# Kernel optimization log

Measured on AMD Instinct MI355X. Metric: run time of the kernel, lower is better.

## Reference

```python
import jax, jax.numpy as jnp
import numpy as np

B, NQ, NK = 4, 1024, 1024
DQ, DK, DO = 1024, 1024, 1024
H = 16
HIDDEN = 2048  # mlp_ratio=2.0


def dyt(x, alpha, gamma):
    # DyT: gamma * tanh(alpha * x), gamma broadcast over last (channel) dim for 3D input
    return gamma[None, None, :] * jnp.tanh(alpha * x)


def setup_inputs() -> dict:
    key = jax.random.key(0)
    ks = jax.random.split(key, 12)
    s = lambda d: 1.0 / np.sqrt(d)
    return {
        "xk": jax.random.normal(ks[0], (B, NK, DK), jnp.float32),
        "xq": jax.random.normal(ks[1], (B, NQ, DQ), jnp.float32),
        "alpha_q": jnp.float32(0.5), "gamma_q": jnp.ones((DQ,), jnp.float32),
        "alpha_k": jnp.float32(0.5), "gamma_k": jnp.ones((DK,), jnp.float32),
        "Wq": jax.random.normal(ks[2], (DQ, DO), jnp.float32) * s(DQ),
        "Wkv": jax.random.normal(ks[3], (DK, 2 * DO), jnp.float32) * s(DK),
        "Wproj": jax.random.normal(ks[4], (DO, DO), jnp.float32) * s(DO),
        "bproj": jnp.zeros((DO,), jnp.float32),
        "alpha2": jnp.float32(0.5), "gamma2": jnp.ones((DO,), jnp.float32),
        "W1": jax.random.normal(ks[5], (DO, HIDDEN), jnp.float32) * s(DO),
        "b1": jnp.zeros((HIDDEN,), jnp.float32),
        "W2": jax.random.normal(ks[6], (HIDDEN, DO), jnp.float32) * s(HIDDEN),
        "b2": jnp.zeros((DO,), jnp.float32),
    }


def reference(xk, xq, alpha_q, gamma_q, alpha_k, gamma_k, Wq, Wkv, Wproj, bproj,
              alpha2, gamma2, W1, b1, W2, b2):
    head_dim = DO // H
    scale = head_dim ** -0.5
    # DyT pre-norms
    xk_n = dyt(xk, alpha_k, gamma_k)
    xq_n = dyt(xq, alpha_q, gamma_q)
    # projections (qkv_bias=False)
    q = (xq_n @ Wq).reshape(B, NQ, H, head_dim)          # bqhd
    kv = (xk_n @ Wkv).reshape(B, NK, 2, H, head_dim)
    k, v = kv[:, :, 0], kv[:, :, 1]                       # bkhd
    attn = jax.nn.softmax(jnp.einsum('bqhd,bkhd->bhqk', q, k) * scale, axis=-1)
    o = jnp.einsum('bhqk,bkhd->bqhd', attn, v).reshape(B, NQ, DO)
    x = o @ Wproj + bproj
    # MLP with residual (drop_path/dropout are identity in eval)
    h = dyt(x, alpha2, gamma2)
    h = jax.nn.gelu(h @ W1 + b1, approximate=False)
    h = h @ W2 + b2
    return x + h
```

## Files before the change

### kernel.cpp

```cpp
#include <hip/hip_runtime.h>
#include <hip/hip_fp16.h>
#include <cstdint>

typedef _Float16 f16x8 __attribute__((ext_vector_type(8)));
typedef _Float16 f16x4 __attribute__((ext_vector_type(4)));
typedef float    f32x4 __attribute__((ext_vector_type(4)));
typedef float    f32x16 __attribute__((ext_vector_type(16)));

__device__ __forceinline__ f32x4 mfma16(f16x8 a, f16x8 b, f32x4 c) {
  return __builtin_amdgcn_mfma_f32_16x16x32_f16(a, b, c, 0, 0, 0);
}
__device__ __forceinline__ f32x16 mfma32(f16x8 a, f16x8 b, f32x16 c) {
  return __builtin_amdgcn_mfma_f32_32x32x16_f16(a, b, c, 0, 0, 0);
}
__device__ __forceinline__ void gload_lds16(const void* g, void* l) {
  __builtin_amdgcn_global_load_lds(
      (const __attribute__((address_space(1))) void*)g,
      (__attribute__((address_space(3))) void*)l, 16, 0, 0);
}
__device__ __forceinline__ unsigned pkrtz(float a, float b) {
  auto h2 = __builtin_amdgcn_cvt_pkrtz(a, b);
  return __builtin_bit_cast(unsigned, h2);
}

__device__ __forceinline__ void wtrans_tile256(
    const float* __restrict__ S, _Float16* __restrict__ D,
    int R, int C, int bx, int by, float sc, float* tle )
{
  int tx = threadIdx.x & 31, ty = threadIdx.x >> 5;
  int x = bx * 32 + tx;
#pragma unroll
  for (int j = 0; j < 4; ++j) {
    int y = by * 32 + ty + j * 8;
    tle[(ty + j * 8) * 33 + tx] = S[(size_t)y * C + x];
  }
  __syncthreads();
  int xo = by * 32 + tx;
#pragma unroll
  for (int j = 0; j < 4; ++j) {
    int yo = bx * 32 + ty + j * 8;
    D[(size_t)yo * R + xo] = (_Float16)(tle[tx * 33 + ty + j * 8] * sc);
  }
}

__global__ __launch_bounds__(256) void prep_kernel(
    const float* __restrict__ Xq, const float* __restrict__ Xk,
    const float* __restrict__ aq, const float* __restrict__ gq,
    const float* __restrict__ ak, const float* __restrict__ gk,
    _Float16* __restrict__ Yq, _Float16* __restrict__ Yk,
    const float* __restrict__ Wq, const float* __restrict__ Wkv,
    _Float16* __restrict__ WqT, _Float16* __restrict__ WkvT)
{
  if (blockIdx.x < 8192) {
    int i = blockIdx.x * 256 + threadIdx.x;
    const float* X; const float* gamma; float a; _Float16* Y;
    if (i < 1048576) { X = Xq; gamma = gq; a = aq[0]; Y = Yq; }
    else { i -= 1048576; X = Xk; gamma = gk; a = ak[0]; Y = Yk; }
    float4 v = ((const float4*)X)[i];
    int c = (i * 4) & 1023;
    f16x4 o;
    o[0] = (_Float16)(gamma[c + 0] * tanhf(a * v.x));
    o[1] = (_Float16)(gamma[c + 1] * tanhf(a * v.y));
    o[2] = (_Float16)(gamma[c + 2] * tanhf(a * v.z));
    o[3] = (_Float16)(gamma[c + 3] * tanhf(a * v.w));
    *(f16x4*)(Y + (size_t)i * 4) = o;
  } else {
    __shared__ float tle[32 * 33];
    int t = blockIdx.x - 8192;
    const float* S; _Float16* D; int R, C; float sc = 1.0f;
    if (t < 1024)      { S = Wq;  D = WqT;  R = 1024; C = 1024; sc = 0.18033688011112042f; }
    else               { S = Wkv; D = WkvT; R = 1024; C = 2048; t -= 1024; }
    const int tilesX = C >> 5;
    wtrans_tile256(S, D, R, C, t % tilesX, t / tilesX, sc, tle);
  }
}

template <int EPI>
__device__ __forceinline__ void gemm_body(
    _Float16* smem,
    const _Float16* __restrict__ A, const _Float16* __restrict__ BT,
    int N, int K, int bm, int bn,
    _Float16* __restrict__ C16, _Float16* __restrict__ X16,
    const float* __restrict__ bias, const float* __restrict__ alpha_p,
    const float* __restrict__ gamma, const _Float16* __restrict__ resid16,
    float* __restrict__ outf)
{
  const int tid = threadIdx.x;
  const int w = tid >> 6, l = tid & 63;
  const int g = l >> 4, r = l & 15;
  const int wm = w >> 1, wn = w & 1;
  const int srow = tid >> 2;
  const int skey = (tid >> 3) & 3;
  const int scol = ((tid & 3) ^ skey) << 3;

  const _Float16* gA = A + (size_t)(bm + srow) * K + scol;
  const _Float16* gB = BT + (size_t)(bn + srow) * K + scol;
  char* dA = (char*)smem + tid * 16;
  char* dB = (char*)smem + 8192 + tid * 16;

  const int rk = (r >> 1) & 3;
  const int gsw = (g ^ rk) << 3;

  f32x4 acc[2][4] = {};
  const int KT = K >> 5;

  auto stage = [&](int buf) {
    gload_lds16(gA, dA + buf * 16384);
    gload_lds16(gB, dB + buf * 16384);
    gA += 32; gB += 32;
  };

  stage(0);
  stage(1);

  int cur = 0;
  for (int kt = 0; kt < KT; ++kt) {
    if (kt < KT - 1) asm volatile("s_waitcnt vmcnt(2) lgkmcnt(0)" ::: "memory");
    else             asm volatile("s_waitcnt vmcnt(0) lgkmcnt(0)" ::: "memory");
    __builtin_amdgcn_s_barrier();
    asm volatile("" ::: "memory");
    if (kt + 2 < KT) { int b2 = cur + 2; if (b2 >= 3) b2 -= 3; stage(b2); }
    const _Float16* Asc = smem + cur * 8192;
    const _Float16* Bsc = Asc + 4096;
    f16x8 af[2], bf[4];
#pragma unroll
    for (int m = 0; m < 2; ++m)
      af[m] = *(const f16x8*)(Asc + (wm * 32 + m * 16 + r) * 32 + gsw);
#pragma unroll
    for (int n = 0; n < 4; ++n)
      bf[n] = *(const f16x8*)(Bsc + (wn * 64 + n * 16 + r) * 32 + gsw);
    __builtin_amdgcn_s_setprio(1);
#pragma unroll
    for (int m = 0; m < 2; ++m)
#pragma unroll
      for (int n = 0; n < 4; ++n)
        acc[m][n] = mfma16(af[m], bf[n], acc[m][n]);
    __builtin_amdgcn_s_setprio(0);
    ++cur; if (cur == 3) cur = 0;
  }

  const int row0 = bm + wm * 32 + 4 * g;
  const int col0 = bn + wn * 64 + r;

  if constexpr (EPI == 5) {
    if (bn < 1024) {
#pragma unroll
      for (int m = 0; m < 2; ++m)
#pragma unroll
        for (int n = 0; n < 4; ++n)
#pragma unroll
          for (int rr = 0; rr < 4; ++rr)
            C16[(size_t)(row0 + m * 16 + rr) * 1024 + col0 + n * 16] =
                (_Float16)acc[m][n][rr];
    } else {
#pragma unroll
      for (int m = 0; m < 2; ++m) {
        const int row = row0 + m * 16;
        const int bq = row >> 10, nk = row & 1023;
#pragma unroll
        for (int n = 0; n < 4; ++n) {
          const int vcol = col0 + n * 16 - 1024;
          f16x4 t;
#pragma unroll
          for (int rr = 0; rr < 4; ++rr) t[rr] = (_Float16)acc[m][n][rr];
          *(f16x4*)(X16 + ((size_t)((bq << 4) + (vcol >> 6)) * 64 + (vcol & 63)) * 1024 + nk) = t;
        }
      }
    }
    return;
  }

#pragma unroll
  for (int m = 0; m < 2; ++m) {
#pragma unroll
    for (int n = 0; n < 4; ++n) {
#pragma unroll
      for (int rr = 0; rr < 4; ++rr) {
        const int row = row0 + m * 16 + rr;
        const int col = col0 + n * 16;
        const size_t idx = (size_t)row * N + col;
        float v = acc[m][n][rr];
        if constexpr (EPI == 0) {
          C16[idx] = (_Float16)v;
        } else if constexpr (EPI == 2) {
          float x = v + bias[col];
          X16[idx] = (_Float16)x;
          C16[idx] = (_Float16)(gamma[col] * tanhf(alpha_p[0] * x));
        } else if constexpr (EPI == 3) {
          float tt = v + bias[col];
          C16[idx] = (_Float16)(0.5f * tt * (1.0f + erff(tt * 0.7071067811865475f)));
        } else {
          outf[idx] = (float)resid16[idx] + v + bias[col];
        }
      }
    }
  }
}

template <int EPI>
__global__ __launch_bounds__(512, 6) void gemm_f16(
    const _Float16* __restrict__ A, const _Float16* __restrict__ BT,
    int N, int K, int nTnShift,
    _Float16* __restrict__ C16, _Float16* __restrict__ X16,
    const float* __restrict__ bias, const float* __restrict__ alpha_p,
    const float* __restrict__ gamma, const _Float16* __restrict__ resid16,
    float* __restrict__ outf)
{
  __shared__ __align__(16) _Float16 smem[24576];
  const int chunk = gridDim.x >> 3;
  const int bid = ((int)blockIdx.x & 7) * chunk + ((int)blockIdx.x >> 3);
  const int bm = (bid >> nTnShift) << 7;
  const int bn = (bid & ((1 << nTnShift) - 1)) << 7;
  gemm_body<EPI>(smem, A, BT, N, K, bm, bn,
                 C16, X16, bias, alpha_p, gamma, resid16, outf);
}

__global__ __launch_bounds__(512, 6) void gemm_qkv(
    const _Float16* __restrict__ Aq, const _Float16* __restrict__ Bq,
    _Float16* __restrict__ Cq,
    const _Float16* __restrict__ Ak, const _Float16* __restrict__ Bk,
    _Float16* __restrict__ K16, _Float16* __restrict__ VT)
{
  __shared__ __align__(16) _Float16 smem[24576];
  int bid = ((int)blockIdx.x & 7) * 96 + ((int)blockIdx.x >> 3);
  if (bid < 256) {
    gemm_body<0>(smem, Aq, Bq, 1024, 1024, (bid >> 3) << 7, (bid & 7) << 7,
                 Cq, nullptr, nullptr, nullptr, nullptr, nullptr, nullptr);
  } else {
    bid -= 256;
    gemm_body<5>(smem, Ak, Bk, 2048, 1024, (bid >> 4) << 7, (bid & 15) << 7,
                 K16, VT, nullptr, nullptr, nullptr, nullptr, nullptr);
  }
}

__global__ __launch_bounds__(256) void attn_kernel(
    const _Float16* __restrict__ Q, const _Float16* __restrict__ K16,
    const _Float16* __restrict__ VT, _Float16* __restrict__ O,
    const float* __restrict__ Wproj, const float* __restrict__ W1,
    const float* __restrict__ W2,
    _Float16* __restrict__ WprojT, _Float16* __restrict__ W1T,
    _Float16* __restrict__ W2T)
{
  __shared__ __align__(16) char smemc[65536];

  const int tid = threadIdx.x;

  if (blockIdx.x >= 512) {
    int t = blockIdx.x - 512;
    const float* S; _Float16* D; int R, C;
    if (t < 1024)      { S = Wproj; D = WprojT; R = 1024; C = 1024; }
    else if (t < 3072) { S = W1;    D = W1T;    R = 1024; C = 2048; t -= 1024; }
    else               { S = W2;    D = W2T;    R = 2048; C = 1024; t -= 3072; }
    const int tilesX = C >> 5;
    wtrans_tile256(S, D, R, C, t % tilesX, t / tilesX, 1.0f, (float*)smemc);
    return;
  }

  const int bid = ((int)blockIdx.x & 7) * 64 + ((int)blockIdx.x >> 3);
  const int qb = bid & 7, hh = (bid >> 3) & 15, b = bid >> 7;
  const int w = tid >> 6, l = tid & 63;
  const int r = l & 31, h2 = l >> 5;
  const int q0 = qb * 128 + w * 32;

  f16x8 qf[4];
  {
    const _Float16* qp = Q + (size_t)(b * 1024 + q0 + r) * 1024 + hh * 64 + 8 * h2;
#pragma unroll
    for (int s = 0; s < 4; ++s) qf[s] = *(const f16x8*)(qp + s * 16);
  }

  f32x16 oacc0 = {}, oacc1 = {};
  float rl0 = 0.f, rl1 = 0.f, rl2 = 0.f, rl3 = 0.f;

  const int srow = tid >> 3, sslot = tid & 7;
  const int swz = (sslot ^ (srow & 7)) << 3;
  const _Float16* kbase = K16 + (size_t)(b * 1024 + srow) * 1024 + hh * 64 + swz;
  const _Float16* vbase = VT + ((size_t)((b * 16 + hh) * 64) + srow) * 1024 + swz;
  char* kd0 = (char*)smemc + tid * 16;
  char* vd0 = (char*)smemc + 8192 + tid * 16;

  auto stage = [&](int t) {
    const size_t kb = (size_t)(t << 6);
    const int buf = t & 3;
    char* kd = kd0 + buf * 16384;
    char* vd = vd0 + buf * 16384;
#pragma unroll
    for (int j = 0; j < 2; ++j)
      gload_lds16(kbase + (kb + 32 * j) * 1024, kd + j * 4096);
#pragma unroll
    for (int j = 0; j < 2; ++j)
      gload_lds16(vbase + (size_t)(32 * j) * 1024 + kb, vd + j * 4096);
  };

  stage(0);
  stage(1);

  const int rsw0 = r & 7;

  for (int kt = 0; kt < 16; ++kt) {
    if (kt + 2 < 16) stage(kt + 2);
    if (kt < 14)       asm volatile("s_waitcnt vmcnt(8)" ::: "memory");
    else if (kt == 14) asm volatile("s_waitcnt vmcnt(4)" ::: "memory");
    else               asm volatile("s_waitcnt vmcnt(0)" ::: "memory");
    __builtin_amdgcn_s_barrier();
    asm volatile("" ::: "memory");

    const _Float16* Kc = (const _Float16*)(smemc + (kt & 3) * 16384);
    const _Float16* Vc = Kc + 4096;

    f32x16 s0 = {}, s1 = {};
    __builtin_amdgcn_s_setprio(1);
#pragma unroll
    for (int s = 0; s < 4; ++s) {
      const int cch = 2 * s + h2;
      f16x8 a0 = *(const f16x8*)(Kc + r * 64 + ((cch ^ rsw0) << 3));
      f16x8 a1 = *(const f16x8*)(Kc + (32 + r) * 64 + ((cch ^ rsw0) << 3));
      s0 = mfma32(a0, qf[s], s0);
      s1 = mfma32(a1, qf[s], s1);
    }
    __builtin_amdgcn_s_setprio(0);

#pragma unroll
    for (int i = 0; i < 16; i += 4) {
      s0[i]   = __builtin_amdgcn_exp2f(s0[i]);   rl0 += s0[i];
      s0[i+1] = __builtin_amdgcn_exp2f(s0[i+1]); rl1 += s0[i+1];
      s0[i+2] = __builtin_amdgcn_exp2f(s0[i+2]); rl2 += s0[i+2];
      s0[i+3] = __builtin_amdgcn_exp2f(s0[i+3]); rl3 += s0[i+3];
    }
#pragma unroll
    for (int i = 0; i < 16; i += 4) {
      s1[i]   = __builtin_amdgcn_exp2f(s1[i]);   rl0 += s1[i];
      s1[i+1] = __builtin_amdgcn_exp2f(s1[i+1]); rl1 += s1[i+1];
      s1[i+2] = __builtin_amdgcn_exp2f(s1[i+2]); rl2 += s1[i+2];
      s1[i+3] = __builtin_amdgcn_exp2f(s1[i+3]); rl3 += s1[i+3];
    }

    unsigned own[16];
#pragma unroll
    for (int u = 0; u < 8; ++u) {
      const int tb = (u & 3) * 4;
      if (u < 4) {
        own[2 * u]     = pkrtz(s0[tb], s0[tb + 1]);
        own[2 * u + 1] = pkrtz(s0[tb + 2], s0[tb + 3]);
      } else {
        own[2 * u]     = pkrtz(s1[tb], s1[tb + 1]);
        own[2 * u + 1] = pkrtz(s1[tb + 2], s1[tb + 3]);
      }
    }
    f16x8 pf[4];
#pragma unroll
    for (int s = 0; s < 4; ++s) {
      auto r0 = __builtin_amdgcn_permlane32_swap(own[4 * s], own[4 * s + 2], false, false);
      auto r1 = __builtin_amdgcn_permlane32_swap(own[4 * s + 1], own[4 * s + 3], false, false);
      union { unsigned u[4]; f16x8 v; } fu;
      fu.u[0] = r0[0]; fu.u[1] = r1[0]; fu.u[2] = r0[1]; fu.u[3] = r1[1];
      pf[s] = fu.v;
    }

    __builtin_amdgcn_s_setprio(1);
#pragma unroll
    for (int s = 0; s < 4; ++s) {
      const int cch = 2 * s + h2;
      f16x8 va = *(const f16x8*)(Vc + r * 64 + ((cch ^ rsw0) << 3));
      f16x8 vb = *(const f16x8*)(Vc + (32 + r) * 64 + ((cch ^ rsw0) << 3));
      oacc0 = mfma32(va, pf[s], oacc0);
      oacc1 = mfma32(vb, pf[s], oacc1);
    }
    __builtin_amdgcn_s_setprio(0);
    asm volatile("" ::: "memory");
  }

  float run_l = (rl0 + rl1) + (rl2 + rl3);
  const float inv = 1.0f / (run_l + __shfl_xor(run_l, 32));
  _Float16* op = O + (size_t)(b * 1024 + q0 + r) * 1024 + hh * 64 + 4 * h2;
#pragma unroll
  for (int u = 0; u < 4; ++u) {
    f16x4 t0, t1;
#pragma unroll
    for (int v = 0; v < 4; ++v) {
      t0[v] = (_Float16)(oacc0[4 * u + v] * inv);
      t1[v] = (_Float16)(oacc1[4 * u + v] * inv);
    }
    *(f16x4*)(op + 8 * u) = t0;
    *(f16x4*)(op + 32 + 8 * u) = t1;
  }
}

extern "C" void kernel_launch(void* const* d_in, const int* in_sizes, int n_in,
                              void* d_out, int out_size, void* d_ws, size_t ws_size,
                              hipStream_t stream)
{
  const float* xk      = (const float*)d_in[0];
  const float* xq      = (const float*)d_in[1];
  const float* alpha_q = (const float*)d_in[2];
  const float* gamma_q = (const float*)d_in[3];
  const float* alpha_k = (const float*)d_in[4];
  const float* gamma_k = (const float*)d_in[5];
  const float* Wq      = (const float*)d_in[6];
  const float* Wkv     = (const float*)d_in[7];
  const float* Wproj   = (const float*)d_in[8];
  const float* bproj   = (const float*)d_in[9];
  const float* alpha2  = (const float*)d_in[10];
  const float* gamma2  = (const float*)d_in[11];
  const float* W1      = (const float*)d_in[12];
  const float* b1      = (const float*)d_in[13];
  const float* W2      = (const float*)d_in[14];
  const float* b2      = (const float*)d_in[15];

  char* p = (char*)d_ws;
  _Float16* xqn    = (_Float16*)p; p += 8388608;
  _Float16* xkn    = (_Float16*)p; p += 8388608;
  _Float16* WqT    = (_Float16*)p; p += 2097152;
  _Float16* WkvT   = (_Float16*)p; p += 4194304;
  _Float16* WprojT = (_Float16*)p; p += 2097152;
  _Float16* W1T    = (_Float16*)p; p += 4194304;
  _Float16* W2T    = (_Float16*)p; p += 4194304;
  _Float16* q16    = (_Float16*)p; p += 8388608;
  _Float16* vt16   = (_Float16*)p; p += 8388608;
  _Float16* k16    = (_Float16*)p; p += 8388608;
  _Float16* h16    = (_Float16*)p; p += 16777216;
  _Float16* o16    = (_Float16*)p; p += 8388608;
  _Float16* x16  = q16;
  _Float16* g16  = xqn;
  float*    outf = (float*)d_out;

  prep_kernel<<<11264, 256, 0, stream>>>(xq, xk, alpha_q, gamma_q, alpha_k, gamma_k,
      xqn, xkn, Wq, Wkv, WqT, WkvT);
  gemm_qkv<<<768, 512, 0, stream>>>(xqn, WqT, q16, xkn, WkvT, k16, vt16);
  attn_kernel<<<5632, 256, 0, stream>>>(q16, k16, vt16, o16,
      Wproj, W1, W2, WprojT, W1T, W2T);
  gemm_f16<2><<<256, 512, 0, stream>>>(o16, WprojT, 1024, 1024, 3,
      g16, x16, bproj, alpha2, gamma2, nullptr, nullptr);
  gemm_f16<3><<<512, 512, 0, stream>>>(g16, W1T, 2048, 1024, 4,
      h16, nullptr, b1, nullptr, nullptr, nullptr, nullptr);
  gemm_f16<4><<<256, 512, 0, stream>>>(h16, W2T, 1024, 2048, 3,
      nullptr, nullptr, b2, nullptr, nullptr, x16, outf);
}
```

Baseline: 159.9 us.

## Compute softmax row sums via MFMA with ones and move weight transposes to prep

The attention kernel drops the per-element VALU accumulation of exponentials into row-sum registers and the final cross-lane shuffle. Instead it runs an extra MFMA per step against a vector of ones, which yields the row sums of the fp16-rounded probabilities. The Wproj/W1/W2 transposes move from trailing blocks of the attention launch into the prep kernel, so the attention launch shrinks to 512 blocks. This trades VALU adds for extra matrix-unit work and makes the prep kernel longer.

```diff
diff --git a/kernel.cpp b/kernel.cpp
--- a/kernel.cpp
+++ b/kernel.cpp
@@ -49,7 +49,11 @@
     const float* __restrict__ ak, const float* __restrict__ gk,
     _Float16* __restrict__ Yq, _Float16* __restrict__ Yk,
     const float* __restrict__ Wq, const float* __restrict__ Wkv,
-    _Float16* __restrict__ WqT, _Float16* __restrict__ WkvT)
+    _Float16* __restrict__ WqT, _Float16* __restrict__ WkvT,
+    const float* __restrict__ Wproj, const float* __restrict__ W1,
+    const float* __restrict__ W2,
+    _Float16* __restrict__ WprojT, _Float16* __restrict__ W1T,
+    _Float16* __restrict__ W2T)
 {
   if (blockIdx.x < 8192) {
     int i = blockIdx.x * 256 + threadIdx.x;
@@ -68,8 +72,11 @@
     __shared__ float tle[32 * 33];
     int t = blockIdx.x - 8192;
     const float* S; _Float16* D; int R, C; float sc = 1.0f;
-    if (t < 1024)      { S = Wq;  D = WqT;  R = 1024; C = 1024; sc = 0.18033688011112042f; }
-    else               { S = Wkv; D = WkvT; R = 1024; C = 2048; t -= 1024; }
+    if (t < 1024)      { S = Wq;    D = WqT;    R = 1024; C = 1024; sc = 0.18033688011112042f; }
+    else if (t < 3072) { S = Wkv;   D = WkvT;   R = 1024; C = 2048; t -= 1024; }
+    else if (t < 4096) { S = Wproj; D = WprojT; R = 1024; C = 1024; t -= 3072; }
+    else if (t < 6144) { S = W1;    D = W1T;    R = 1024; C = 2048; t -= 4096; }
+    else               { S = W2;    D = W2T;    R = 2048; C = 1024; t -= 6144; }
     const int tilesX = C >> 5;
     wtrans_tile256(S, D, R, C, t % tilesX, t / tilesX, sc, tle);
   }
@@ -235,26 +242,11 @@
 
 __global__ __launch_bounds__(256) void attn_kernel(
     const _Float16* __restrict__ Q, const _Float16* __restrict__ K16,
-    const _Float16* __restrict__ VT, _Float16* __restrict__ O,
-    const float* __restrict__ Wproj, const float* __restrict__ W1,
-    const float* __restrict__ W2,
-    _Float16* __restrict__ WprojT, _Float16* __restrict__ W1T,
-    _Float16* __restrict__ W2T)
+    const _Float16* __restrict__ VT, _Float16* __restrict__ O)
 {
   __shared__ __align__(16) char smemc[65536];
 
   const int tid = threadIdx.x;
-
-  if (blockIdx.x >= 512) {
-    int t = blockIdx.x - 512;
-    const float* S; _Float16* D; int R, C;
-    if (t < 1024)      { S = Wproj; D = WprojT; R = 1024; C = 1024; }
-    else if (t < 3072) { S = W1;    D = W1T;    R = 1024; C = 2048; t -= 1024; }
-    else               { S = W2;    D = W2T;    R = 2048; C = 1024; t -= 3072; }
-    const int tilesX = C >> 5;
-    wtrans_tile256(S, D, R, C, t % tilesX, t / tilesX, 1.0f, (float*)smemc);
-    return;
-  }
 
   const int bid = ((int)blockIdx.x & 7) * 64 + ((int)blockIdx.x >> 3);
   const int qb = bid & 7, hh = (bid >> 3) & 15, b = bid >> 7;
@@ -269,8 +261,11 @@
     for (int s = 0; s < 4; ++s) qf[s] = *(const f16x8*)(qp + s * 16);
   }
 
-  f32x16 oacc0 = {}, oacc1 = {};
-  float rl0 = 0.f, rl1 = 0.f, rl2 = 0.f, rl3 = 0.f;
+  f16x8 onef;
+#pragma unroll
+  for (int i = 0; i < 8; ++i) onef[i] = (_Float16)1.0f;
+
+  f32x16 oacc0 = {}, oacc1 = {}, lacc = {};
 
   const int srow = tid >> 3, sslot = tid & 7;
   const int swz = (sslot ^ (srow & 7)) << 3;
@@ -321,19 +316,9 @@
     __builtin_amdgcn_s_setprio(0);
 
 #pragma unroll
-    for (int i = 0; i < 16; i += 4) {
-      s0[i]   = __builtin_amdgcn_exp2f(s0[i]);   rl0 += s0[i];
-      s0[i+1] = __builtin_amdgcn_exp2f(s0[i+1]); rl1 += s0[i+1];
-      s0[i+2] = __builtin_amdgcn_exp2f(s0[i+2]); rl2 += s0[i+2];
-      s0[i+3] = __builtin_amdgcn_exp2f(s0[i+3]); rl3 += s0[i+3];
-    }
-#pragma unroll
-    for (int i = 0; i < 16; i += 4) {
-      s1[i]   = __builtin_amdgcn_exp2f(s1[i]);   rl0 += s1[i];
-      s1[i+1] = __builtin_amdgcn_exp2f(s1[i+1]); rl1 += s1[i+1];
-      s1[i+2] = __builtin_amdgcn_exp2f(s1[i+2]); rl2 += s1[i+2];
-      s1[i+3] = __builtin_amdgcn_exp2f(s1[i+3]); rl3 += s1[i+3];
-    }
+    for (int i = 0; i < 16; ++i) s0[i] = __builtin_amdgcn_exp2f(s0[i]);
+#pragma unroll
+    for (int i = 0; i < 16; ++i) s1[i] = __builtin_amdgcn_exp2f(s1[i]);
 
     unsigned own[16];
 #pragma unroll
@@ -365,13 +350,13 @@
       f16x8 vb = *(const f16x8*)(Vc + (32 + r) * 64 + ((cch ^ rsw0) << 3));
       oacc0 = mfma32(va, pf[s], oacc0);
       oacc1 = mfma32(vb, pf[s], oacc1);
+      lacc  = mfma32(onef, pf[s], lacc);
     }
     __builtin_amdgcn_s_setprio(0);
     asm volatile("" ::: "memory");
   }
 
-  float run_l = (rl0 + rl1) + (rl2 + rl3);
-  const float inv = 1.0f / (run_l + __shfl_xor(run_l, 32));
+  const float inv = 1.0f / lacc[0];
   _Float16* op = O + (size_t)(b * 1024 + q0 + r) * 1024 + hh * 64 + 4 * h2;
 #pragma unroll
   for (int u = 0; u < 4; ++u) {
@@ -424,11 +409,10 @@
   _Float16* g16  = xqn;
   float*    outf = (float*)d_out;
 
-  prep_kernel<<<11264, 256, 0, stream>>>(xq, xk, alpha_q, gamma_q, alpha_k, gamma_k,
-      xqn, xkn, Wq, Wkv, WqT, WkvT);
+  prep_kernel<<<16384, 256, 0, stream>>>(xq, xk, alpha_q, gamma_q, alpha_k, gamma_k,
+      xqn, xkn, Wq, Wkv, WqT, WkvT, Wproj, W1, W2, WprojT, W1T, W2T);
   gemm_qkv<<<768, 512, 0, stream>>>(xqn, WqT, q16, xkn, WkvT, k16, vt16);
-  attn_kernel<<<5632, 256, 0, stream>>>(q16, k16, vt16, o16,
-      Wproj, W1, W2, WprojT, W1T, W2T);
+  attn_kernel<<<512, 256, 0, stream>>>(q16, k16, vt16, o16);
   gemm_f16<2><<<256, 512, 0, stream>>>(o16, WprojT, 1024, 1024, 3,
       g16, x16, bproj, alpha2, gamma2, nullptr, nullptr);
   gemm_f16<3><<<512, 512, 0, stream>>>(g16, W1T, 2048, 1024, 4,
```

Result: no change. 160.0 us (median of 2 runs) (+0.1%).
